# Performance work log

Hardware: AMD Instinct MI355X
Metric: run time of the kernel (lower is better)

The kernel has to match this reference:

```python
import jax, jax.numpy as jnp
import numpy as np

MARGIN = 0.5
B, C, P, N = 32768, 64, 16, 48  # problems, candidates/problem, max pos, max neg


def setup_inputs() -> dict:
    key = jax.random.key(0)
    k0, k1, k2, k3, k4 = jax.random.split(key, 5)
    return {
        "scores": jax.random.normal(k0, (B * C,), dtype=jnp.float32),
        "pos_indices": jax.random.randint(k1, (B, P), 0, C, dtype=jnp.int32),
        "neg_indices": jax.random.randint(k2, (B, N), 0, C, dtype=jnp.int32),
        "pos_counts": jax.random.randint(k3, (B,), 0, P + 1, dtype=jnp.int32),
        "neg_counts": jax.random.randint(k4, (B,), 0, N + 1, dtype=jnp.int32),
    }


def reference(scores, pos_indices, neg_indices, pos_counts, neg_counts):
    b, p = pos_indices.shape
    n = neg_indices.shape[1]
    c = scores.shape[0] // b
    # per-problem offsets into the flat score vector (uniform candidate_counts = c)
    offs = (jnp.arange(b, dtype=jnp.int32) * c)[:, None]
    pos = scores[offs + pos_indices]  # [B, P]
    neg = scores[offs + neg_indices]  # [B, N]
    # ragged validity masks (count == 0 reproduces the skip for empty lists)
    pos_mask = (jnp.arange(p, dtype=jnp.int32)[None, :] < pos_counts[:, None])
    neg_mask = (jnp.arange(n, dtype=jnp.int32)[None, :] < neg_counts[:, None])
    pair_mask = (pos_mask[:, :, None] & neg_mask[:, None, :]).astype(scores.dtype)  # [B,P,N]
    # relu(margin - pos + neg) over every pos x neg pair within each problem
    pair_loss = jax.nn.relu(MARGIN - pos[:, :, None] + neg[:, None, :])
    total = jnp.sum(pair_loss * pair_mask)
    count = jnp.sum(pair_mask)
    return jnp.where(count > 0, total / jnp.maximum(count, 1.0), jnp.array(0.0, scores.dtype))
```

## Files before the change

kernel.cpp:

```cpp
#include <hip/hip_runtime.h>


#define MARGIN 0.5f

constexpr int C = 64;
constexpr int P = 16;
constexpr int N = 48;
constexpr int BLOCK = 256;
constexpr int WAVES_PER_BLOCK = BLOCK / 64;
constexpr int PROBS_PER_WAVE = 4;
constexpr int PROBS_PER_BLOCK = WAVES_PER_BLOCK * PROBS_PER_WAVE;

__global__ __launch_bounds__(BLOCK) void mpcl_partial_kernel(
    const float* __restrict__ scores,
    const int*   __restrict__ pos_indices,
    const int*   __restrict__ neg_indices,
    const int*   __restrict__ pos_counts,
    const int*   __restrict__ neg_counts,
    float2*      __restrict__ partials,
    int B)
{
    const int lane = threadIdx.x & 63;
    const int wave = threadIdx.x >> 6;

    float tot = 0.0f;
    float cnt = 0.0f;

    const int b0 = (blockIdx.x * WAVES_PER_BLOCK + wave) * PROBS_PER_WAVE;

    for (int k = 0; k < PROBS_PER_WAVE; ++k) {
        const int b = b0 + k;
        if (b >= B) break;

        const int pc = pos_counts[b];
        const int nc = neg_counts[b];

        float myval  = 0.0f;
        float negval = -1e30f;
        if (lane >= 48) {
            const int idx = pos_indices[b * P + (lane - 48)];
            myval = scores[b * C + idx];
        } else if (lane < nc) {
            const int idx = neg_indices[b * N + lane];
            negval = scores[b * C + idx];
        }

        float s = 0.0f;
        for (int i = 0; i < pc; ++i) {
            const float pos_i = __shfl(myval, 48 + i);
            s += fmaxf(MARGIN - pos_i + negval, 0.0f);
        }
        tot += s;
        cnt += (float)(pc * nc);
    }

    #pragma unroll
    for (int off = 32; off; off >>= 1) tot += __shfl_xor(tot, off);

    __shared__ float2 lds[WAVES_PER_BLOCK];
    if (lane == 0) lds[wave] = make_float2(tot, cnt);
    __syncthreads();

    if (threadIdx.x == 0) {
        float2 acc = lds[0];
        #pragma unroll
        for (int w = 1; w < WAVES_PER_BLOCK; ++w) { acc.x += lds[w].x; acc.y += lds[w].y; }
        partials[blockIdx.x] = acc;
    }
}

__global__ __launch_bounds__(BLOCK) void mpcl_final_kernel(
    const float2* __restrict__ partials, int n, float* __restrict__ out)
{
    float tot = 0.0f, cnt = 0.0f;
    for (int i = threadIdx.x; i < n; i += BLOCK) {
        const float2 p = partials[i];
        tot += p.x;
        cnt += p.y;
    }
    #pragma unroll
    for (int off = 32; off; off >>= 1) {
        tot += __shfl_xor(tot, off);
        cnt += __shfl_xor(cnt, off);
    }

    __shared__ float2 lds[WAVES_PER_BLOCK];
    const int wave = threadIdx.x >> 6;
    const int lane = threadIdx.x & 63;
    if (lane == 0) lds[wave] = make_float2(tot, cnt);
    __syncthreads();

    if (threadIdx.x == 0) {
        float T = 0.0f, Cn = 0.0f;
        #pragma unroll
        for (int w = 0; w < WAVES_PER_BLOCK; ++w) { T += lds[w].x; Cn += lds[w].y; }
        out[0] = (Cn > 0.0f) ? (T / fmaxf(Cn, 1.0f)) : 0.0f;
    }
}

extern "C" void kernel_launch(void* const* d_in, const int* in_sizes, int n_in,
                              void* d_out, int out_size, void* d_ws, size_t ws_size,
                              hipStream_t stream) {
    const float* scores      = (const float*)d_in[0];
    const int*   pos_indices = (const int*)d_in[1];
    const int*   neg_indices = (const int*)d_in[2];
    const int*   pos_counts  = (const int*)d_in[3];
    const int*   neg_counts  = (const int*)d_in[4];
    float*       out         = (float*)d_out;

    const int B = in_sizes[3];
    const int grid = (B + PROBS_PER_BLOCK - 1) / PROBS_PER_BLOCK;

    float2* partials = (float2*)d_ws;

    mpcl_partial_kernel<<<grid, BLOCK, 0, stream>>>(
        scores, pos_indices, neg_indices, pos_counts, neg_counts, partials, B);
    mpcl_final_kernel<<<1, BLOCK, 0, stream>>>(partials, grid, out);
}
```

Baseline: 81.67 us.

## Batch-load scores rows and use readlane with fully unrolled pair loop

```diff
diff --git a/kernel.cpp b/kernel.cpp
--- a/kernel.cpp
+++ b/kernel.cpp
@@ -11,6 +11,10 @@
 constexpr int PROBS_PER_WAVE = 4;
 constexpr int PROBS_PER_BLOCK = WAVES_PER_BLOCK * PROBS_PER_WAVE;
 
+__device__ __forceinline__ float readlane_f(float v, int l) {
+    return __uint_as_float(__builtin_amdgcn_readlane(__float_as_uint(v), l));
+}
+
 __global__ __launch_bounds__(BLOCK) void mpcl_partial_kernel(
     const float* __restrict__ scores,
     const int*   __restrict__ pos_indices,
@@ -22,36 +26,63 @@
 {
     const int lane = threadIdx.x & 63;
     const int wave = threadIdx.x >> 6;
+    const int b0 = (blockIdx.x * WAVES_PER_BLOCK + wave) * PROBS_PER_WAVE;
 
     float tot = 0.0f;
     float cnt = 0.0f;
 
-    const int b0 = (blockIdx.x * WAVES_PER_BLOCK + wave) * PROBS_PER_WAVE;
-
-    for (int k = 0; k < PROBS_PER_WAVE; ++k) {
-        const int b = b0 + k;
-        if (b >= B) break;
-
-        const int pc = pos_counts[b];
-        const int nc = neg_counts[b];
-
-        float myval  = 0.0f;
-        float negval = -1e30f;
-        if (lane >= 48) {
-            const int idx = pos_indices[b * P + (lane - 48)];
-            myval = scores[b * C + idx];
-        } else if (lane < nc) {
-            const int idx = neg_indices[b * N + lane];
-            negval = scores[b * C + idx];
+    if (b0 + PROBS_PER_WAVE <= B) {
+        int   pc[PROBS_PER_WAVE], nc[PROBS_PER_WAVE], idx[PROBS_PER_WAVE];
+        float sc[PROBS_PER_WAVE];
+        #pragma unroll
+        for (int k = 0; k < PROBS_PER_WAVE; ++k) {
+            const int b = b0 + k;
+            pc[k] = pos_counts[b];
+            nc[k] = neg_counts[b];
+            idx[k] = (lane >= 48)
+                ? pos_indices[(size_t)b * P + (lane - 48)]
+                : neg_indices[(size_t)b * N + lane];
+            sc[k] = scores[(size_t)b * C + lane];
         }
 
-        float s = 0.0f;
-        for (int i = 0; i < pc; ++i) {
-            const float pos_i = __shfl(myval, 48 + i);
-            s += fmaxf(MARGIN - pos_i + negval, 0.0f);
+        #pragma unroll
+        for (int k = 0; k < PROBS_PER_WAVE; ++k) {
+            const float val  = __shfl(sc[k], idx[k]);
+            const float negv = (lane < nc[k]) ? val : -1e30f;
+            const float posv = (lane >= 48 && (lane - 48) < pc[k]) ? val : 1e30f;
+            const float mneg = MARGIN + negv;
+
+            float s = 0.0f;
+            #pragma unroll
+            for (int i = 0; i < P; ++i) {
+                s += fmaxf(mneg - readlane_f(posv, 48 + i), 0.0f);
+            }
+            tot += s;
+            cnt += (float)(pc[k] * nc[k]);
         }
-        tot += s;
-        cnt += (float)(pc * nc);
+    } else {
+        for (int k = 0; k < PROBS_PER_WAVE; ++k) {
+            const int b = b0 + k;
+            if (b >= B) break;
+            const int pc = pos_counts[b];
+            const int nc = neg_counts[b];
+            float myval  = 0.0f;
+            float negval = -1e30f;
+            if (lane >= 48) {
+                const int idx = pos_indices[(size_t)b * P + (lane - 48)];
+                myval = scores[(size_t)b * C + idx];
+            } else if (lane < nc) {
+                const int idx = neg_indices[(size_t)b * N + lane];
+                negval = scores[(size_t)b * C + idx];
+            }
+            float s = 0.0f;
+            for (int i = 0; i < pc; ++i) {
+                const float pos_i = __shfl(myval, 48 + i);
+                s += fmaxf(MARGIN - pos_i + negval, 0.0f);
+            }
+            tot += s;
+            cnt += (float)(pc * nc);
+        }
     }
 
     #pragma unroll
```

New measurement: 77.33 us. 5.3% less time.
